# Kernel optimization log

Hardware: AMD Instinct MI355X
Metric: run time of the kernel (lower is better)

Reference implementation:

```python
import jax, jax.numpy as jnp
import numpy as np


def setup_inputs() -> dict:
    key = jax.random.key(0)
    kx, ky = jax.random.split(key)
    B, N, M, D = 4, 4096, 4096, 128
    xd = jax.random.normal(kx, (B, N, D), dtype=jnp.float32)
    yd = jax.random.normal(ky, (B, M, D), dtype=jnp.float32)
    mask = jnp.ones((B, N, M), dtype=jnp.float32)
    return {"xd": xd, "yd": yd, "mask": mask}


def _pairwise_l2(x, y):
    # x: (B, N, D), y: (B, M, D) -> (B, N, M) euclidean distances
    x2 = jnp.sum(x * x, axis=-1)[:, :, None]          # (B, N, 1)
    y2 = jnp.sum(y * y, axis=-1)[:, None, :]          # (B, 1, M)
    xy = jnp.einsum("bnd,bmd->bnm", x, y)             # (B, N, M)
    d2 = jnp.maximum(x2 + y2 - 2.0 * xy, 0.0)
    return jnp.sqrt(d2)


def reference(xd, yd, mask):
    # NNDFMatcher.forward: orientation='x', smallest=True, topk=None
    dists = _pairwise_l2(xd, yd) * mask               # (B, N, M)
    pairs = jnp.argmin(dists, axis=-1)                # (B, N) int
    top_dists = jnp.min(dists, axis=-1)               # (B, N)
    M = mask.shape[-1]
    # one-hot scatter: match_mask[b, n, pairs[b, n]] = 1
    match_mask = (pairs[..., None] == jnp.arange(M)[None, None, :]).astype(mask.dtype)
    return match_mask, pairs, top_dists
```

## Files before the change

kernel.cpp:

```cpp
#include <hip/hip_runtime.h>


typedef float  f32x4   __attribute__((ext_vector_type(4)));
typedef float  f32x16  __attribute__((ext_vector_type(16)));
typedef short  bf16x8  __attribute__((ext_vector_type(8)));

#define PS ((size_t)2097152)

#define WAITVM_(N) asm volatile("s_waitcnt vmcnt(" #N ")" ::: "memory")
#define WAITVM(N)  WAITVM_(N)
#define BAR        __builtin_amdgcn_s_barrier()
#define FENCE      asm volatile("" ::: "memory")

__device__ __forceinline__ unsigned short f2bf(float x) {
    unsigned u = __float_as_uint(x);
    u += 0x7FFFu + ((u >> 16) & 1u);
    return (unsigned short)(u >> 16);
}
__device__ __forceinline__ float bf2f(unsigned short s) {
    return __uint_as_float(((unsigned)s) << 16);
}
__device__ __forceinline__ void gload_lds16(const void* g, void* l) {
    __builtin_amdgcn_global_load_lds(
        (const __attribute__((address_space(1))) void*)g,
        (__attribute__((address_space(3))) void*)l, 16, 0, 0);
}

__global__ __launch_bounds__(256) void k_prep(const float* __restrict__ xd,
                                              const float* __restrict__ yd,
                                              unsigned short* __restrict__ pl,
                                              float* __restrict__ ws) {
    __shared__ float sm[4][16];
    int bid  = blockIdx.x;
    int i    = bid >> 10;
    int b    = (bid >> 8) & 3;
    int rblk = bid & 255;
    int tid  = threadIdx.x;
    int kb   = tid >> 6;
    int l    = tid & 63;
    int lg4  = (l >> 4) & 3;
    int r    = rblk * 16 + (l & 15);
    int k0   = kb * 32 + lg4 * 8;
    const float* src = (i ? yd : xd) + ((size_t)(b * 4096 + r) * 128 + k0);
    float v[8];
    *reinterpret_cast<float4*>(v)     = *reinterpret_cast<const float4*>(src);
    *reinterpret_cast<float4*>(v + 4) = *reinterpret_cast<const float4*>(src + 4);
    bf16x8 hv, mv, lv;
    float s = 0.f;
    #pragma unroll
    for (int e = 0; e < 8; ++e) {
        float x = v[e];
        s = fmaf(x, x, s);
        unsigned short h  = f2bf(x);
        float r1 = x - bf2f(h);
        unsigned short m  = f2bf(r1);
        float r2 = r1 - bf2f(m);
        unsigned short lo = f2bf(r2);
        hv[e] = (short)h; mv[e] = (short)m; lv[e] = (short)lo;
    }
    int kh   = kb >> 1;
    int kc2  = (kb & 1) * 2 + (lg4 >> 1);
    int land = (r & 31) + ((lg4 & 1) << 5);
    size_t base = ((size_t)((b * 2 + kh) * 128 + (rblk >> 1))) * 2048
                + (size_t)(kc2 * 64 + land) * 8;
    unsigned short* dst = pl + (size_t)(i * 3) * PS;
    *reinterpret_cast<bf16x8*>(dst + base)          = hv;
    *reinterpret_cast<bf16x8*>(dst + base + PS)     = mv;
    *reinterpret_cast<bf16x8*>(dst + base + 2 * PS) = lv;
    s += __shfl_xor(s, 16);
    s += __shfl_xor(s, 32);
    if (l < 16) sm[kb][l] = s;
    __syncthreads();
    if (tid < 16) {
        float t = sm[0][tid] + sm[1][tid] + sm[2][tid] + sm[3][tid];
        ws[(i ? 16384 : 0) + b * 4096 + rblk * 16 + tid] = t;
    }
}

__global__ __launch_bounds__(256, 2) void k_gemm(const float* __restrict__ mask,
                                                 const float* __restrict__ ws,
                                                 const unsigned short* __restrict__ pl,
                                                 float* __restrict__ out,
                                                 float* __restrict__ pv,
                                                 int* __restrict__ pi) {
    __shared__ __align__(16) unsigned short Ab[2][2][4096];
    __shared__ __align__(16) unsigned short Bp[2][3][4096];

    const int bid = blockIdx.x;
    const int xcd = bid & 7;
    const int b   = xcd >> 1;
    const int ch  = xcd & 1;
    const int rt  = bid >> 3;
    const int tid = threadIdx.x;
    const int w   = tid >> 6, l = tid & 63;
    const int wr  = w >> 1, wc = w & 1;
    const int l31 = l & 31, lg1 = l >> 5;
    const int g0  = b * 4096 + rt * 64;

    float x2r[16];
    #pragma unroll
    for (int rg = 0; rg < 16; ++rg)
        x2r[rg] = ws[g0 + wr * 32 + (rg & 3) + 8 * (rg >> 2) + 4 * lg1];

    const float* y2g = ws + 16384 + b * 4096 + ch * 2048 + wc * 32 + l31;

    #pragma unroll
    for (int kh = 0; kh < 2; ++kh)
        #pragma unroll
        for (int ap = 0; ap < 2; ++ap) {
            const unsigned short* Ac = pl + (size_t)ap * PS
                + (((size_t)((b * 2 + kh) * 128 + rt * 2)) << 11);
            gload_lds16((const char*)Ac + tid * 16,
                        (char*)(&Ab[kh][ap][0]) + tid * 16);
            gload_lds16((const char*)Ac + 4096 + tid * 16,
                        (char*)(&Ab[kh][ap][0]) + 4096 + tid * 16);
        }
    bf16x8 Al[2][4];
    #pragma unroll
    for (int kh = 0; kh < 2; ++kh) {
        const unsigned short* Ac = pl + (size_t)2 * PS
            + (((size_t)((b * 2 + kh) * 128 + rt * 2 + wr)) << 11);
        #pragma unroll
        for (int kc = 0; kc < 4; ++kc)
            Al[kh][kc] = *reinterpret_cast<const bf16x8*>(Ac + (kc * 64 + l) * 8);
    }

#define STAGE_B(CT, KH, SLOT) do {                                                \
    _Pragma("unroll") for (int bp_ = 0; bp_ < 3; ++bp_) {                         \
        const unsigned short* Bc_ = pl + (size_t)(3 + bp_) * PS                   \
            + (((size_t)((b * 2 + (KH)) * 128 + ch * 64 + (CT) * 2)) << 11);      \
        gload_lds16((const char*)Bc_ + tid * 16,                                  \
                    (char*)(&Bp[SLOT][bp_][0]) + tid * 16);                       \
        gload_lds16((const char*)Bc_ + 4096 + tid * 16,                           \
                    (char*)(&Bp[SLOT][bp_][0]) + 4096 + tid * 16);                \
    }                                                                             \
} while (0)

#define MLOAD16(CT) do {                                                          \
    _Pragma("unroll") for (int K = 0; K < 16; ++K) {                              \
        const int row_ = wr * 32 + (K & 3) + 8 * (K >> 2) + 4 * lg1;              \
        pm[K] = mask[(size_t)(g0 + row_) * 4096                                   \
                     + (ch * 2048 + (CT) * 64 + wc * 32 + l31)];                  \
    }                                                                             \
    yv = y2g[(CT) * 64];                                                          \
} while (0)

#define ZST(CT, I) do {                                                           \
    const f32x4 z_ = (f32x4){0.f, 0.f, 0.f, 0.f};                                 \
    *reinterpret_cast<f32x4*>(out + (size_t)(g0 + (I) * 16 + (tid >> 4)) * 4096   \
        + ch * 2048 + (CT) * 64 + ((tid & 15) << 2)) = z_;                        \
} while (0)

#define COMPUTE(KH, SLOT) do {                                                    \
    __builtin_amdgcn_s_setprio(1);                                                \
    _Pragma("unroll") for (int kc = 0; kc < 4; ++kc) {                            \
        const int fa = wr * 2048 + kc * 512 + l * 8;                              \
        bf16x8 Ah_ = *reinterpret_cast<const bf16x8*>(&Ab[KH][0][fa]);            \
        bf16x8 Am_ = *reinterpret_cast<const bf16x8*>(&Ab[KH][1][fa]);            \
        bf16x8 Al_ = Al[KH][kc];                                                  \
        const int fb = wc * 2048 + kc * 512 + l * 8;                              \
        bf16x8 Bh_ = *reinterpret_cast<const bf16x8*>(&Bp[SLOT][0][fb]);          \
        bf16x8 Bm_ = *reinterpret_cast<const bf16x8*>(&Bp[SLOT][1][fb]);          \
        bf16x8 Bl_ = *reinterpret_cast<const bf16x8*>(&Bp[SLOT][2][fb]);          \
        acc = __builtin_amdgcn_mfma_f32_32x32x16_bf16(Ah_, Bh_, acc, 0, 0, 0);    \
        acc = __builtin_amdgcn_mfma_f32_32x32x16_bf16(Am_, Bh_, acc, 0, 0, 0);    \
        acc = __builtin_amdgcn_mfma_f32_32x32x16_bf16(Al_, Bh_, acc, 0, 0, 0);    \
        acc = __builtin_amdgcn_mfma_f32_32x32x16_bf16(Ah_, Bm_, acc, 0, 0, 0);    \
        acc = __builtin_amdgcn_mfma_f32_32x32x16_bf16(Am_, Bm_, acc, 0, 0, 0);    \
        acc = __builtin_amdgcn_mfma_f32_32x32x16_bf16(Ah_, Bl_, acc, 0, 0, 0);    \
    }                                                                             \
    __builtin_amdgcn_s_setprio(0);                                                \
} while (0)

    float pm[16], yv;
    f32x16 acc;

    STAGE_B(0, 0, 0);
    WAITVM(0);
    BAR;

    const double INITD = __hiloint2double(0x7f7fffff, 0);
    double bv[16];
    #pragma unroll
    for (int q = 0; q < 16; ++q) bv[q] = INITD;

    #pragma unroll 1
    for (int ct = 0; ct < 32; ++ct) {
        const int ctn = (ct < 31) ? ct + 1 : 31;

        WAITVM(2); BAR;
        #pragma unroll
        for (int e = 0; e < 16; ++e) acc[e] = 0.f;
        STAGE_B(ct, 1, 1);
        FENCE;
        MLOAD16(ct);
        FENCE;
        ZST(ct, 0); ZST(ct, 1);
        COMPUTE(0, 0);

        WAITVM(18); BAR;
        STAGE_B(ctn, 0, 0);
        FENCE;
        ZST(ct, 2); ZST(ct, 3);
        COMPUTE(1, 1);

        {
            const int c = ch * 2048 + ct * 64 + wc * 32 + l31;
            #pragma unroll
            for (int rg = 0; rg < 16; ++rg) {
                float d2 = fmaf(acc[rg], -2.0f, x2r[rg]) + yv;
                float d  = sqrtf(fmaxf(d2, 0.0f)) * pm[rg];
                double pk = __hiloint2double(__float_as_int(d), c);
                bv[rg] = fmin(bv[rg], pk);
            }
        }
    }
#undef STAGE_B
#undef MLOAD16
#undef ZST
#undef COMPUTE

    WAITVM(0);

    #pragma unroll
    for (int off = 1; off < 32; off <<= 1) {
        #pragma unroll
        for (int q = 0; q < 16; ++q)
            bv[q] = fmin(bv[q], __shfl_xor(bv[q], off));
    }
    __syncthreads();
    double* cd = reinterpret_cast<double*>(&Bp[0][0][0]);
    if (l31 == 0) {
        #pragma unroll
        for (int rg = 0; rg < 16; ++rg) {
            int rowl = wr * 32 + (rg & 3) + 8 * (rg >> 2) + 4 * lg1;
            cd[rowl * 2 + wc] = bv[rg];
        }
    }
    __syncthreads();
    if (tid < 64) {
        double v = fmin(cd[tid * 2], cd[tid * 2 + 1]);
        int grow = g0 + tid;
        pv[grow * 2 + ch] = __int_as_float(__double2hiint(v));
        pi[grow * 2 + ch] = __double2loint(v);
    }
}

__global__ __launch_bounds__(256) void k_fin(const float* __restrict__ pv,
                                             const int* __restrict__ pi,
                                             float* __restrict__ out) {
    int t = blockIdx.x * 256 + threadIdx.x;
    float v0 = pv[t * 2], v1 = pv[t * 2 + 1];
    int   i0 = pi[t * 2], i1 = pi[t * 2 + 1];
    bool take1 = (v1 < v0) || (v1 == v0 && i1 < i0);
    float v  = take1 ? v1 : v0;
    int   ix = take1 ? i1 : i0;
    out[67108864 + t]         = (float)ix;
    out[67108864 + 16384 + t] = v;
    out[(size_t)t * 4096 + (size_t)ix] = 1.0f;
}

__global__ __launch_bounds__(256) void k_rowsq(const float* __restrict__ xd,
                                               const float* __restrict__ yd,
                                               float* __restrict__ ws) {
    int tid  = threadIdx.x;
    int wid  = tid >> 6, lane = tid & 63;
    int gr   = blockIdx.x * 4 + wid;
    const float* src = (gr < 16384) ? (xd + (size_t)gr * 128)
                                    : (yd + (size_t)(gr - 16384) * 128);
    float2 v = reinterpret_cast<const float2*>(src)[lane];
    float s  = v.x * v.x + v.y * v.y;
    for (int off = 32; off > 0; off >>= 1) s += __shfl_down(s, off);
    if (lane == 0) ws[gr] = s;
}

__global__ __launch_bounds__(256, 1) void k_main_fb(const float* __restrict__ xd,
                                                    const float* __restrict__ yd,
                                                    const float* __restrict__ mask,
                                                    const float* __restrict__ ws,
                                                    float* __restrict__ pvals,
                                                    int* __restrict__ pidx,
                                                    float* __restrict__ mm) {
    __shared__ __align__(16) float Xs[128 * 128];
    __shared__ __align__(16) float Ys[128 * 128];
    const int bid  = blockIdx.x;
    const int mh   = bid & 1;
    const int rb   = (bid >> 1) & 31;
    const int b    = bid >> 6;
    const int tid  = threadIdx.x;
    const int ty   = tid >> 4;
    const int tx   = tid & 15;
    const int row0 = rb * 128;
    const int m0   = mh * 2048;
    {
        const float4 z = make_float4(0.f, 0.f, 0.f, 0.f);
        size_t base = ((size_t)(b * 4096 + row0)) * 4096 + (size_t)m0;
        for (int r = 0; r < 128; ++r) {
            float4* p = reinterpret_cast<float4*>(mm + base + (size_t)r * 4096);
            p[tid] = z; p[tid + 256] = z;
        }
    }
    {
        int lrow = tid >> 5, slot = tid & 31;
        for (int p = 0; p < 16; ++p) {
            int row  = p * 8 + lrow;
            float4 v = reinterpret_cast<const float4*>(
                           xd + ((size_t)(b * 4096 + row0 + row)) * 128)[slot];
            int ss = slot ^ (row & 31);
            *reinterpret_cast<float4*>(&Xs[row * 128 + (ss << 2)]) = v;
        }
    }
    float x2r[8];
    #pragma unroll
    for (int i = 0; i < 8; ++i) x2r[i] = ws[b * 4096 + row0 + ty * 8 + i];
    const float* y2g = ws + 16384 + b * 4096;
    float bv[8]; int bi[8];
    #pragma unroll
    for (int i = 0; i < 8; ++i) { bv[i] = 3.4e38f; bi[i] = 0; }
    __syncthreads();
    for (int tile = 0; tile < 16; ++tile) {
        const int mbase = m0 + tile * 128;
        {
            int lrow = tid >> 5, slot = tid & 31;
            for (int p = 0; p < 16; ++p) {
                int row  = p * 8 + lrow;
                float4 v = reinterpret_cast<const float4*>(
                               yd + ((size_t)(b * 4096 + mbase + row)) * 128)[slot];
                int ss = slot ^ (row & 31);
                *reinterpret_cast<float4*>(&Ys[row * 128 + (ss << 2)]) = v;
            }
        }
        __syncthreads();
        float acc[8][8];
        #pragma unroll
        for (int i = 0; i < 8; ++i)
            #pragma unroll
            for (int jj = 0; jj < 8; ++jj) acc[i][jj] = 0.0f;
        #pragma unroll 4
        for (int ks = 0; ks < 32; ++ks) {
            float4 bf[8];
            #pragma unroll
            for (int jj = 0; jj < 8; ++jj) {
                int c = jj * 16 + tx;
                bf[jj] = *reinterpret_cast<const float4*>(&Ys[c * 128 + ((ks ^ (c & 31)) << 2)]);
            }
            #pragma unroll
            for (int i = 0; i < 8; ++i) {
                int r = ty * 8 + i;
                float4 a = *reinterpret_cast<const float4*>(&Xs[r * 128 + ((ks ^ (r & 31)) << 2)]);
                #pragma unroll
                for (int jj = 0; jj < 8; ++jj) {
                    acc[i][jj] = fmaf(a.x, bf[jj].x, acc[i][jj]);
                    acc[i][jj] = fmaf(a.y, bf[jj].y, acc[i][jj]);
                    acc[i][jj] = fmaf(a.z, bf[jj].z, acc[i][jj]);
                    acc[i][jj] = fmaf(a.w, bf[jj].w, acc[i][jj]);
                }
            }
        }
        float y2v[8];
        #pragma unroll
        for (int jj = 0; jj < 8; ++jj) y2v[jj] = y2g[mbase + jj * 16 + tx];
        #pragma unroll
        for (int i = 0; i < 8; ++i) {
            int r = ty * 8 + i;
            const float* mr = mask + ((size_t)(b * 4096 + row0 + r)) * 4096;
            #pragma unroll
            for (int jj = 0; jj < 8; ++jj) {
                int   m  = mbase + jj * 16 + tx;
                float d2 = x2r[i] + y2v[jj] - 2.0f * acc[i][jj];
                float d  = sqrtf(fmaxf(d2, 0.0f)) * mr[m];
                if (d < bv[i]) { bv[i] = d; bi[i] = m; }
            }
        }
        __syncthreads();
    }
    float* candv = Xs;
    int*   candi = reinterpret_cast<int*>(Xs + 2048);
    #pragma unroll
    for (int i = 0; i < 8; ++i) {
        int r = ty * 8 + i;
        candv[r * 16 + tx] = bv[i];
        candi[r * 16 + tx] = bi[i];
    }
    __syncthreads();
    if (tid < 128) {
        int   r  = tid;
        float v  = candv[r * 16];
        int   ix = candi[r * 16];
        for (int t = 1; t < 16; ++t) {
            float v2 = candv[r * 16 + t];
            int   i2 = candi[r * 16 + t];
            if (v2 < v || (v2 == v && i2 < ix)) { v = v2; ix = i2; }
        }
        int grow = b * 4096 + row0 + r;
        pvals[grow * 2 + mh] = v;
        pidx [grow * 2 + mh] = ix;
    }
}

__global__ __launch_bounds__(256) void k_fin_fb(const float* __restrict__ pvals,
                                                const int* __restrict__ pidx,
                                                float* __restrict__ out) {
    int t = blockIdx.x * 256 + threadIdx.x;
    float v0 = pvals[t * 2], v1 = pvals[t * 2 + 1];
    int   i0 = pidx [t * 2], i1 = pidx [t * 2 + 1];
    bool take1 = (v1 < v0) || (v1 == v0 && i1 < i0);
    float v  = take1 ? v1 : v0;
    int   ix = take1 ? i1 : i0;
    out[67108864 + t]         = (float)ix;
    out[67108864 + 16384 + t] = v;
    out[(size_t)t * 4096 + (size_t)ix] = 1.0f;
}

extern "C" void kernel_launch(void* const* d_in, const int* in_sizes, int n_in,
                              void* d_out, int out_size, void* d_ws, size_t ws_size,
                              hipStream_t stream) {
    const float* xd   = (const float*)d_in[0];
    const float* yd   = (const float*)d_in[1];
    const float* mask = (const float*)d_in[2];
    float* out = (float*)d_out;
    float* wsf = (float*)d_ws;

    const size_t need = 131072 + 6 * PS * 2 + 262144;
    if (ws_size >= need) {
        unsigned short* pl = (unsigned short*)((char*)d_ws + 131072);
        float* pv = (float*)((char*)d_ws + 131072 + 6 * PS * 2);
        int*   pi = (int*)  ((char*)d_ws + 131072 + 6 * PS * 2 + 131072);
        k_prep <<<2048, 256, 0, stream>>>(xd, yd, pl, wsf);
        k_gemm <<<512,  256, 0, stream>>>(mask, wsf, pl, out, pv, pi);
        k_fin  <<<64,   256, 0, stream>>>(pv, pi, out);
    } else {
        float* pvals = wsf + 32768;
        int*   pidx  = (int*)(wsf + 65536);
        k_rowsq  <<<8192, 256, 0, stream>>>(xd, yd, wsf);
        k_main_fb<<<256,  256, 0, stream>>>(xd, yd, mask, wsf, pvals, pidx, out);
        k_fin_fb <<<64,   256, 0, stream>>>(pvals, pidx, out);
    }
}
```

Baseline: 179.0 us.

## Retile GEMM so each wave owns 32 rows with A fragments in registers

Each block now covers 128 rows by a 1024-column quarter, and each of the four waves keeps all three bf16 split planes of its 32-row A slice in registers. Only B tiles, both K halves in one stage, are streamed through double-buffered LDS. The per-iteration loop is simplified to one stage, compute and epilogue, and the LDS cross-wave reduction is removed. Partial minima go out per column quarter, and the finalize kernel merges four candidates instead of two. This trades more A-register pressure for less LDS A traffic and fewer barriers.

```diff
diff --git a/kernel.cpp b/kernel.cpp
--- a/kernel.cpp
+++ b/kernel.cpp
@@ -83,99 +83,101 @@
                                                  float* __restrict__ out,
                                                  float* __restrict__ pv,
                                                  int* __restrict__ pi) {
-    __shared__ __align__(16) unsigned short Ab[2][2][4096];
-    __shared__ __align__(16) unsigned short Bp[2][3][4096];
+    __shared__ __align__(16) unsigned short Bp[2][2][3][2048];
 
     const int bid = blockIdx.x;
     const int xcd = bid & 7;
     const int b   = xcd >> 1;
-    const int ch  = xcd & 1;
-    const int rt  = bid >> 3;
+    const int cqh = xcd & 1;
+    const int sub = bid >> 3;
+    const int cq  = cqh * 2 + (sub & 1);
+    const int rt  = sub >> 1;
     const int tid = threadIdx.x;
     const int w   = tid >> 6, l = tid & 63;
-    const int wr  = w >> 1, wc = w & 1;
     const int l31 = l & 31, lg1 = l >> 5;
-    const int g0  = b * 4096 + rt * 64;
+    const int g0  = b * 4096 + rt * 128;
+    const int col0 = cq * 1024;
+
+    bf16x8 Af[3][2][4];
+    #pragma unroll
+    for (int p = 0; p < 3; ++p)
+        #pragma unroll
+        for (int kh = 0; kh < 2; ++kh) {
+            const unsigned short* Ac = pl + (size_t)p * PS
+                + (((size_t)((b * 2 + kh) * 128 + rt * 4 + w)) << 11);
+            #pragma unroll
+            for (int kc = 0; kc < 4; ++kc)
+                Af[p][kh][kc] = *reinterpret_cast<const bf16x8*>(Ac + (kc * 64 + l) * 8);
+        }
 
     float x2r[16];
     #pragma unroll
     for (int rg = 0; rg < 16; ++rg)
-        x2r[rg] = ws[g0 + wr * 32 + (rg & 3) + 8 * (rg >> 2) + 4 * lg1];
-
-    const float* y2g = ws + 16384 + b * 4096 + ch * 2048 + wc * 32 + l31;
-
-    #pragma unroll
-    for (int kh = 0; kh < 2; ++kh)
-        #pragma unroll
-        for (int ap = 0; ap < 2; ++ap) {
-            const unsigned short* Ac = pl + (size_t)ap * PS
-                + (((size_t)((b * 2 + kh) * 128 + rt * 2)) << 11);
-            gload_lds16((const char*)Ac + tid * 16,
-                        (char*)(&Ab[kh][ap][0]) + tid * 16);
-            gload_lds16((const char*)Ac + 4096 + tid * 16,
-                        (char*)(&Ab[kh][ap][0]) + 4096 + tid * 16);
-        }
-    bf16x8 Al[2][4];
-    #pragma unroll
-    for (int kh = 0; kh < 2; ++kh) {
-        const unsigned short* Ac = pl + (size_t)2 * PS
-            + (((size_t)((b * 2 + kh) * 128 + rt * 2 + wr)) << 11);
-        #pragma unroll
-        for (int kc = 0; kc < 4; ++kc)
-            Al[kh][kc] = *reinterpret_cast<const bf16x8*>(Ac + (kc * 64 + l) * 8);
-    }
-
-#define STAGE_B(CT, KH, SLOT) do {                                                \
-    _Pragma("unroll") for (int bp_ = 0; bp_ < 3; ++bp_) {                         \
-        const unsigned short* Bc_ = pl + (size_t)(3 + bp_) * PS                   \
-            + (((size_t)((b * 2 + (KH)) * 128 + ch * 64 + (CT) * 2)) << 11);      \
+        x2r[rg] = ws[g0 + w * 32 + (rg & 3) + 8 * (rg >> 2) + 4 * lg1];
+
+    const unsigned mbase = (unsigned)(g0 + w * 32 + 4 * lg1) * 4096u
+                         + (unsigned)(col0 + l31);
+    const unsigned ybase = 16384u + (unsigned)(b * 4096 + col0 + l31);
+    const unsigned zbase = (unsigned)(g0 + (tid >> 3)) * 4096u
+                         + (unsigned)(col0 + ((tid & 7) << 2));
+
+#define STAGE(CT, SLOT) do {                                                      \
+    _Pragma("unroll") for (int kh_ = 0; kh_ < 2; ++kh_)                           \
+    _Pragma("unroll") for (int p_ = 0; p_ < 3; ++p_) {                            \
+        const unsigned short* Bc_ = pl + (size_t)(3 + p_) * PS                    \
+            + (((size_t)((b * 2 + kh_) * 128 + cq * 32 + (CT))) << 11);           \
         gload_lds16((const char*)Bc_ + tid * 16,                                  \
-                    (char*)(&Bp[SLOT][bp_][0]) + tid * 16);                       \
-        gload_lds16((const char*)Bc_ + 4096 + tid * 16,                           \
-                    (char*)(&Bp[SLOT][bp_][0]) + 4096 + tid * 16);                \
+                    (char*)(&Bp[SLOT][kh_][p_][0]) + tid * 16);                   \
     }                                                                             \
 } while (0)
 
-#define MLOAD16(CT) do {                                                          \
-    _Pragma("unroll") for (int K = 0; K < 16; ++K) {                              \
-        const int row_ = wr * 32 + (K & 3) + 8 * (K >> 2) + 4 * lg1;              \
-        pm[K] = mask[(size_t)(g0 + row_) * 4096                                   \
-                     + (ch * 2048 + (CT) * 64 + wc * 32 + l31)];                  \
+#define MLOAD(CT) do {                                                            \
+    const unsigned mb_ = mbase + (unsigned)((CT) * 32);                           \
+    _Pragma("unroll") for (int rg_ = 0; rg_ < 16; ++rg_) {                        \
+        const unsigned ro_ = (unsigned)(((rg_ & 3) + 8 * (rg_ >> 2)) * 4096);     \
+        pm[rg_] = mask[mb_ + ro_];                                                \
     }                                                                             \
-    yv = y2g[(CT) * 64];                                                          \
+    yv = ws[ybase + (unsigned)((CT) * 32)];                                       \
 } while (0)
 
 #define ZST(CT, I) do {                                                           \
     const f32x4 z_ = (f32x4){0.f, 0.f, 0.f, 0.f};                                 \
-    *reinterpret_cast<f32x4*>(out + (size_t)(g0 + (I) * 16 + (tid >> 4)) * 4096   \
-        + ch * 2048 + (CT) * 64 + ((tid & 15) << 2)) = z_;                        \
+    *reinterpret_cast<f32x4*>(out + zbase                                         \
+        + (unsigned)((I) * 32 * 4096 + (CT) * 32)) = z_;                          \
 } while (0)
 
-#define COMPUTE(KH, SLOT) do {                                                    \
+#define COMPUTE(SLOT) do {                                                        \
     __builtin_amdgcn_s_setprio(1);                                                \
-    _Pragma("unroll") for (int kc = 0; kc < 4; ++kc) {                            \
-        const int fa = wr * 2048 + kc * 512 + l * 8;                              \
-        bf16x8 Ah_ = *reinterpret_cast<const bf16x8*>(&Ab[KH][0][fa]);            \
-        bf16x8 Am_ = *reinterpret_cast<const bf16x8*>(&Ab[KH][1][fa]);            \
-        bf16x8 Al_ = Al[KH][kc];                                                  \
-        const int fb = wc * 2048 + kc * 512 + l * 8;                              \
-        bf16x8 Bh_ = *reinterpret_cast<const bf16x8*>(&Bp[SLOT][0][fb]);          \
-        bf16x8 Bm_ = *reinterpret_cast<const bf16x8*>(&Bp[SLOT][1][fb]);          \
-        bf16x8 Bl_ = *reinterpret_cast<const bf16x8*>(&Bp[SLOT][2][fb]);          \
-        acc = __builtin_amdgcn_mfma_f32_32x32x16_bf16(Ah_, Bh_, acc, 0, 0, 0);    \
-        acc = __builtin_amdgcn_mfma_f32_32x32x16_bf16(Am_, Bh_, acc, 0, 0, 0);    \
-        acc = __builtin_amdgcn_mfma_f32_32x32x16_bf16(Al_, Bh_, acc, 0, 0, 0);    \
-        acc = __builtin_amdgcn_mfma_f32_32x32x16_bf16(Ah_, Bm_, acc, 0, 0, 0);    \
-        acc = __builtin_amdgcn_mfma_f32_32x32x16_bf16(Am_, Bm_, acc, 0, 0, 0);    \
-        acc = __builtin_amdgcn_mfma_f32_32x32x16_bf16(Ah_, Bl_, acc, 0, 0, 0);    \
+    _Pragma("unroll") for (int kh_ = 0; kh_ < 2; ++kh_)                           \
+    _Pragma("unroll") for (int kc_ = 0; kc_ < 4; ++kc_) {                         \
+        const int fb_ = (kc_ * 64 + l) * 8;                                       \
+        bf16x8 Bh_ = *reinterpret_cast<const bf16x8*>(&Bp[SLOT][kh_][0][fb_]);    \
+        bf16x8 Bm_ = *reinterpret_cast<const bf16x8*>(&Bp[SLOT][kh_][1][fb_]);    \
+        bf16x8 Bl_ = *reinterpret_cast<const bf16x8*>(&Bp[SLOT][kh_][2][fb_]);    \
+        acc = __builtin_amdgcn_mfma_f32_32x32x16_bf16(Af[0][kh_][kc_], Bh_, acc, 0, 0, 0); \
+        acc = __builtin_amdgcn_mfma_f32_32x32x16_bf16(Af[1][kh_][kc_], Bh_, acc, 0, 0, 0); \
+        acc = __builtin_amdgcn_mfma_f32_32x32x16_bf16(Af[2][kh_][kc_], Bh_, acc, 0, 0, 0); \
+        acc = __builtin_amdgcn_mfma_f32_32x32x16_bf16(Af[0][kh_][kc_], Bm_, acc, 0, 0, 0); \
+        acc = __builtin_amdgcn_mfma_f32_32x32x16_bf16(Af[1][kh_][kc_], Bm_, acc, 0, 0, 0); \
+        acc = __builtin_amdgcn_mfma_f32_32x32x16_bf16(Af[0][kh_][kc_], Bl_, acc, 0, 0, 0); \
     }                                                                             \
     __builtin_amdgcn_s_setprio(0);                                                \
 } while (0)
 
+#define EPI(CT) do {                                                              \
+    const int c_ = col0 + (CT) * 32 + l31;                                        \
+    _Pragma("unroll") for (int rg_ = 0; rg_ < 16; ++rg_) {                        \
+        float d2 = fmaf(acc[rg_], -2.0f, x2r[rg_]) + yv;                          \
+        float d  = sqrtf(fmaxf(d2, 0.0f)) * pm[rg_];                              \
+        double pk = __hiloint2double(__float_as_int(d), c_);                      \
+        bv[rg_] = fmin(bv[rg_], pk);                                              \
+    }                                                                             \
+} while (0)
+
     float pm[16], yv;
     f32x16 acc;
 
-    STAGE_B(0, 0, 0);
+    STAGE(0, 0);
     WAITVM(0);
     BAR;
 
@@ -188,37 +190,22 @@
     for (int ct = 0; ct < 32; ++ct) {
         const int ctn = (ct < 31) ? ct + 1 : 31;
 
-        WAITVM(2); BAR;
+        WAITVM(4); BAR;
         #pragma unroll
         for (int e = 0; e < 16; ++e) acc[e] = 0.f;
-        STAGE_B(ct, 1, 1);
+        MLOAD(ct);
         FENCE;
-        MLOAD16(ct);
+        STAGE(ctn, (ct + 1) & 1);
         FENCE;
-        ZST(ct, 0); ZST(ct, 1);
-        COMPUTE(0, 0);
-
-        WAITVM(18); BAR;
-        STAGE_B(ctn, 0, 0);
-        FENCE;
-        ZST(ct, 2); ZST(ct, 3);
-        COMPUTE(1, 1);
-
-        {
-            const int c = ch * 2048 + ct * 64 + wc * 32 + l31;
-            #pragma unroll
-            for (int rg = 0; rg < 16; ++rg) {
-                float d2 = fmaf(acc[rg], -2.0f, x2r[rg]) + yv;
-                float d  = sqrtf(fmaxf(d2, 0.0f)) * pm[rg];
-                double pk = __hiloint2double(__float_as_int(d), c);
-                bv[rg] = fmin(bv[rg], pk);
-            }
-        }
-    }
-#undef STAGE_B
-#undef MLOAD16
+        ZST(ct, 0); ZST(ct, 1); ZST(ct, 2); ZST(ct, 3);
+        COMPUTE(ct & 1);
+        EPI(ct);
+    }
+#undef STAGE
+#undef MLOAD
 #undef ZST
 #undef COMPUTE
+#undef EPI
 
     WAITVM(0);
 
@@ -228,21 +215,13 @@
         for (int q = 0; q < 16; ++q)
             bv[q] = fmin(bv[q], __shfl_xor(bv[q], off));
     }
-    __syncthreads();
-    double* cd = reinterpret_cast<double*>(&Bp[0][0][0]);
     if (l31 == 0) {
         #pragma unroll
         for (int rg = 0; rg < 16; ++rg) {
-            int rowl = wr * 32 + (rg & 3) + 8 * (rg >> 2) + 4 * lg1;
-            cd[rowl * 2 + wc] = bv[rg];
-        }
-    }
-    __syncthreads();
-    if (tid < 64) {
-        double v = fmin(cd[tid * 2], cd[tid * 2 + 1]);
-        int grow = g0 + tid;
-        pv[grow * 2 + ch] = __int_as_float(__double2hiint(v));
-        pi[grow * 2 + ch] = __double2loint(v);
+            int grow = g0 + w * 32 + (rg & 3) + 8 * (rg >> 2) + 4 * lg1;
+            pv[grow * 4 + cq] = __int_as_float(__double2hiint(bv[rg]));
+            pi[grow * 4 + cq] = __double2loint(bv[rg]);
+        }
     }
 }
 
@@ -250,11 +229,14 @@
                                              const int* __restrict__ pi,
                                              float* __restrict__ out) {
     int t = blockIdx.x * 256 + threadIdx.x;
-    float v0 = pv[t * 2], v1 = pv[t * 2 + 1];
-    int   i0 = pi[t * 2], i1 = pi[t * 2 + 1];
-    bool take1 = (v1 < v0) || (v1 == v0 && i1 < i0);
-    float v  = take1 ? v1 : v0;
-    int   ix = take1 ? i1 : i0;
+    float v  = pv[t * 4];
+    int   ix = pi[t * 4];
+    #pragma unroll
+    for (int q = 1; q < 4; ++q) {
+        float v2 = pv[t * 4 + q];
+        int   i2 = pi[t * 4 + q];
+        if (v2 < v || (v2 == v && i2 < ix)) { v = v2; ix = i2; }
+    }
     out[67108864 + t]         = (float)ix;
     out[67108864 + 16384 + t] = v;
     out[(size_t)t * 4096 + (size_t)ix] = 1.0f;
@@ -421,11 +403,11 @@
     float* out = (float*)d_out;
     float* wsf = (float*)d_ws;
 
-    const size_t need = 131072 + 6 * PS * 2 + 262144;
+    const size_t need = 131072 + 6 * PS * 2 + 524288;
     if (ws_size >= need) {
         unsigned short* pl = (unsigned short*)((char*)d_ws + 131072);
         float* pv = (float*)((char*)d_ws + 131072 + 6 * PS * 2);
-        int*   pi = (int*)  ((char*)d_ws + 131072 + 6 * PS * 2 + 131072);
+        int*   pi = (int*)  ((char*)d_ws + 131072 + 6 * PS * 2 + 262144);
         k_prep <<<2048, 256, 0, stream>>>(xd, yd, pl, wsf);
         k_gemm <<<512,  256, 0, stream>>>(mask, wsf, pl, out, pv, pi);
         k_fin  <<<64,   256, 0, stream>>>(pv, pi, out);
```

After: 179.2 us, median of 2. Within noise of the previous version (+0.1%).
